# Performance work log

Measured on AMD Instinct MI355X. Metric: run time of the kernel, lower is better.

Reference implementation:

```python
import jax, jax.numpy as jnp
import numpy as np

EPS = 1e-8  # torch cosine_similarity norm clamp

def _cos(a, b, axis=-1):
    na = jnp.maximum(jnp.linalg.norm(a, axis=axis), EPS)
    nb = jnp.maximum(jnp.linalg.norm(b, axis=axis), EPS)
    return jnp.sum(a * b, axis=axis) / (na * nb)

def setup_inputs() -> dict:
    key = jax.random.key(0)
    ks = jax.random.split(key, 9)
    B, L, D, S = 8, 8192, 512, 131072
    scale = 0.02
    x = jax.random.normal(ks[0], (B, L, D), jnp.float32)
    context_W = jax.random.normal(ks[1], (D, D), jnp.float32) * scale
    context_b = jnp.zeros((D,), jnp.float32)
    pred_W1 = jax.random.normal(ks[2], (D, D), jnp.float32) * scale
    pred_b1 = jnp.zeros((D,), jnp.float32)
    pred_W2 = jax.random.normal(ks[3], (D, D), jnp.float32) * scale
    pred_b2 = jnp.zeros((D,), jnp.float32)
    raw_embeddings = jax.random.normal(ks[4], (S, D), jnp.float32)
    u = jax.random.uniform(ks[5], (S,), jnp.float32)
    surprise_level = jnp.where(u > 0.5, u, 0.0)  # ~half the slots active
    return {"x": x, "context_W": context_W, "context_b": context_b,
            "pred_W1": pred_W1, "pred_b1": pred_b1,
            "pred_W2": pred_W2, "pred_b2": pred_b2,
            "raw_embeddings": raw_embeddings, "surprise_level": surprise_level}

def reference(x, context_W, context_b, pred_W1, pred_b1, pred_W2, pred_b2,
              raw_embeddings, surprise_level):
    # context = pad(x[:, :-1], left-shift by one along seq), i.e. causal previous token
    context = jnp.pad(x[:, :-1, :], ((0, 0), (1, 0), (0, 0)))
    # predictor MLP on projected context (torch Linear: y = x @ W.T + b)
    ctx = context @ context_W.T + context_b
    h = jax.nn.gelu(ctx @ pred_W1.T + pred_b1, approximate=False)
    prediction = h @ pred_W2.T + pred_b2  # [B, L, D]
    mse = jnp.mean((x - prediction) ** 2, axis=-1)
    prediction_surprise = jnp.sqrt(mse)  # [B, L]

    # memory-contrastive surprise: cosine sim of pooled x vs active stored embeddings
    active = surprise_level > 0  # [S]
    x_pooled = jnp.mean(x, axis=1)  # [B, D]
    sim = _cos(x_pooled[:, None, :], raw_embeddings[None, :, :])  # [B, S]
    sim = jnp.where(active[None, :], sim, -jnp.inf)
    max_sim = jnp.max(sim, axis=-1)           # [B]
    best_idx = jnp.argmax(sim, axis=-1)       # [B]
    best_stored = raw_embeddings[best_idx]    # [B, D] argmax-based gather
    divergence = 1.0 - _cos(x, best_stored[:, None, :])  # [B, L]
    pattern_match = (max_sim[:, None] > 0.3).astype(x.dtype)
    contrastive = pattern_match * divergence

    surprise = jnp.maximum(prediction_surprise, contrastive * 2.0)  # [B, L]
    return surprise
```

## Files before the change

kernel.cpp:

```cpp
#include <hip/hip_runtime.h>
#include <math.h>

#define OFF_SIMKEY   0
#define OFF_POOLED   1024
#define ZEROED_BYTES 17408
#define OFF_MAXSIM   17408
#define OFF_NORME    17664
#define OFF_EBEST    17920
#define OFF_BPRIME   34304
#define OFF_WP       36864
#define OFF_W2B      561152

typedef __attribute__((ext_vector_type(8))) short bf16x8;
typedef __attribute__((ext_vector_type(4))) float f32x4;

__device__ inline unsigned short f2bf(float f) {
    unsigned int u = __float_as_uint(f);
    unsigned int r = (u + 0x7FFFu + ((u >> 16) & 1u)) >> 16;
    return (unsigned short)r;
}

__device__ inline void load_lds_16(const void* g, void* l) {
    __builtin_amdgcn_global_load_lds((const __attribute__((address_space(1))) void*)g,
                                     (__attribute__((address_space(3))) void*)l, 16, 0, 0);
}

__global__ void __launch_bounds__(256) k_pre(const float* __restrict__ W1, const float* __restrict__ Wc,
                      const float* __restrict__ b1, const float* __restrict__ bc,
                      unsigned short* __restrict__ Wp, float* __restrict__ bprime) {
    __shared__ float w1row[512];
    __shared__ float wsum[4];
    int t = threadIdx.x;
    int n = blockIdx.x >> 1, half = blockIdx.x & 1;
    if (t < 128) ((float4*)w1row)[t] = ((const float4*)(W1 + (size_t)n * 512))[t];
    __syncthreads();
    int k = half * 256 + t;
    float acc = 0.f;
#pragma unroll 8
    for (int j = 0; j < 512; ++j) acc += w1row[j] * Wc[(size_t)j * 512 + k];
    Wp[(size_t)n * 512 + k] = f2bf(acc);
    if (half == 0) {
        float p = w1row[t] * bc[t] + w1row[t + 256] * bc[t + 256];
#pragma unroll
        for (int m = 32; m >= 1; m >>= 1) p += __shfl_xor(p, m);
        if ((t & 63) == 0) wsum[t >> 6] = p;
        __syncthreads();
        if (t == 0) bprime[n] = b1[n] + wsum[0] + wsum[1] + wsum[2] + wsum[3];
    }
}

__global__ void __launch_bounds__(256) k_cast(const float* __restrict__ W2, unsigned short* __restrict__ W2b) {
    int i = blockIdx.x * 1024 + threadIdx.x * 4;
    float4 v = *(const float4*)(W2 + i);
    ushort4 o;
    o.x = f2bf(v.x); o.y = f2bf(v.y); o.z = f2bf(v.z); o.w = f2bf(v.w);
    *(ushort4*)(W2b + i) = o;
}

__global__ void __launch_bounds__(512) k_pool(const float* __restrict__ x, float* __restrict__ pooled) {
    int d = threadIdx.x;
    int b = blockIdx.y;
    int l0 = blockIdx.x * 128;
    const float* p = x + ((size_t)b * 8192 + l0) * 512 + d;
    float s = 0.f;
    for (int i = 0; i < 128; ++i) s += p[(size_t)i * 512];
    atomicAdd(&pooled[b * 512 + d], s);
}

__global__ void __launch_bounds__(256) k_sim(const float* __restrict__ E, const float* __restrict__ sl,
                     const float* __restrict__ pooledws, unsigned long long* __restrict__ simkey) {
    __shared__ float ps[4096];
    __shared__ unsigned long long wkey[4][8];
    int t = threadIdx.x, lane = t & 63, w = t >> 6;
#pragma unroll
    for (int c = 0; c < 16; ++c) ps[t + c * 256] = pooledws[t + c * 256] * (1.0f / 8192.0f);
    __syncthreads();
    float pr[8][8];
#pragma unroll
    for (int b = 0; b < 8; ++b) {
        float4 v0 = *(const float4*)&ps[b * 512 + lane * 8];
        float4 v1 = *(const float4*)&ps[b * 512 + lane * 8 + 4];
        pr[b][0] = v0.x; pr[b][1] = v0.y; pr[b][2] = v0.z; pr[b][3] = v0.w;
        pr[b][4] = v1.x; pr[b][5] = v1.y; pr[b][6] = v1.z; pr[b][7] = v1.w;
    }
    float npinv[8];
#pragma unroll
    for (int b = 0; b < 8; ++b) {
        float s = 0.f;
#pragma unroll
        for (int j = 0; j < 8; ++j) s += pr[b][j] * pr[b][j];
#pragma unroll
        for (int m = 32; m >= 1; m >>= 1) s += __shfl_xor(s, m);
        npinv[b] = 1.0f / fmaxf(sqrtf(s), 1e-8f);
    }
    unsigned long long best[8];
#pragma unroll
    for (int b = 0; b < 8; ++b) best[b] = 0ull;
    int sbase = blockIdx.x * 64 + w * 16;
    float mysl = (lane < 16) ? sl[sbase + lane] : 0.f;
    unsigned long long mask = __ballot(mysl > 0.0f);
    for (int it = 0; it < 16; ++it) {
        if (!((mask >> it) & 1ull)) continue;
        int s = sbase + it;
        const float4* ep = (const float4*)(E + (size_t)s * 512);
        float4 e0 = ep[lane * 2], e1 = ep[lane * 2 + 1];
        float nrm = e0.x * e0.x + e0.y * e0.y + e0.z * e0.z + e0.w * e0.w
                  + e1.x * e1.x + e1.y * e1.y + e1.z * e1.z + e1.w * e1.w;
        float dt[8];
#pragma unroll
        for (int b = 0; b < 8; ++b)
            dt[b] = e0.x * pr[b][0] + e0.y * pr[b][1] + e0.z * pr[b][2] + e0.w * pr[b][3]
                  + e1.x * pr[b][4] + e1.y * pr[b][5] + e1.z * pr[b][6] + e1.w * pr[b][7];
#pragma unroll
        for (int m = 32; m >= 1; m >>= 1) {
            nrm += __shfl_xor(nrm, m);
#pragma unroll
            for (int b = 0; b < 8; ++b) dt[b] += __shfl_xor(dt[b], m);
        }
        float neinv = 1.0f / fmaxf(sqrtf(nrm), 1e-8f);
#pragma unroll
        for (int b = 0; b < 8; ++b) {
            float sim = dt[b] * npinv[b] * neinv;
            unsigned int u = __float_as_uint(sim);
            unsigned int k32 = (u & 0x80000000u) ? ~u : (u | 0x80000000u);
            unsigned long long key = ((unsigned long long)k32 << 32) | (unsigned int)(~(unsigned int)s);
            if (key > best[b]) best[b] = key;
        }
    }
    if (lane == 0) {
#pragma unroll
        for (int b = 0; b < 8; ++b) wkey[w][b] = best[b];
    }
    __syncthreads();
    if (t < 8) {
        unsigned long long k = wkey[0][t];
#pragma unroll
        for (int w2 = 1; w2 < 4; ++w2) if (wkey[w2][t] > k) k = wkey[w2][t];
        if (k) atomicMax(&simkey[t], k);
    }
}

__global__ void __launch_bounds__(64) k_b2(const float* __restrict__ E, const unsigned long long* __restrict__ simkey,
                    float* __restrict__ max_sim, float* __restrict__ norm_e, float* __restrict__ ebest) {
    int b = blockIdx.x, lane = threadIdx.x;
    unsigned long long key = simkey[b];
    float ms; unsigned int idx;
    if (key == 0ull) { ms = -1e30f; idx = 0u; }
    else {
        unsigned int k32 = (unsigned int)(key >> 32);
        unsigned int u = (k32 & 0x80000000u) ? (k32 & 0x7FFFFFFFu) : ~k32;
        ms = __uint_as_float(u);
        idx = ~(unsigned int)(key & 0xFFFFFFFFull);
    }
    const float4* ep = (const float4*)(E + (size_t)idx * 512);
    float4 e0 = ep[lane * 2], e1 = ep[lane * 2 + 1];
    *(float4*)&ebest[b * 512 + lane * 8] = e0;
    *(float4*)&ebest[b * 512 + lane * 8 + 4] = e1;
    float s = e0.x * e0.x + e0.y * e0.y + e0.z * e0.z + e0.w * e0.w
            + e1.x * e1.x + e1.y * e1.y + e1.z * e1.z + e1.w * e1.w;
#pragma unroll
    for (int m = 32; m >= 1; m >>= 1) s += __shfl_xor(s, m);
    if (lane == 0) { max_sim[b] = ms; norm_e[b] = fmaxf(sqrtf(s), 1e-8f); }
}

__global__ void __launch_bounds__(256, 2) k_fused(
        const float* __restrict__ x, const unsigned short* __restrict__ Wp,
        const float* __restrict__ bprime, const unsigned short* __restrict__ W2b,
        const float* __restrict__ b2, const float* __restrict__ ebest,
        const float* __restrict__ max_sim, const float* __restrict__ norm_e,
        float* __restrict__ out) {
    __shared__ char smem[32768];
    unsigned short* Ts   = (unsigned short*)smem;
    unsigned short* Bs   = (unsigned short*)(smem + 5120);
    unsigned short* hbuf = (unsigned short*)(smem + 13312);
    float* red           = (float*)(smem + 30720);
    int t = threadIdx.x, lane = t & 63, w = t >> 6, l15 = lane & 15, quad = lane >> 4;
    int wr = w >> 1, wc = w & 1;
    const int gr0 = blockIdx.x * 64;
    const int b = gr0 >> 13;
    const int row0 = t >> 3, f4 = t & 7;

    ushort4 ush[16][2];
#pragma unroll
    for (int c = 0; c < 2; ++c) {
        int gr = gr0 + row0 + c * 32;
        bool z = ((gr & 8191) == 0);
        const float* src = x + ((size_t)gr - 1) * 512 + f4 * 4;
#pragma unroll
        for (int kt = 0; kt < 16; ++kt) {
            float4 v = make_float4(0.f, 0.f, 0.f, 0.f);
            if (!z) v = *(const float4*)(src + kt * 32);
            ushort4 o;
            o.x = f2bf(v.x); o.y = f2bf(v.y); o.z = f2bf(v.z); o.w = f2bf(v.w);
            ush[kt][c] = o;
        }
    }

    ushort4 hregs[16][2];
#pragma unroll
    for (int cb = 0; cb < 4; ++cb) {
        f32x4 acc[2][4];
#pragma unroll
        for (int i = 0; i < 2; ++i)
#pragma unroll
            for (int j = 0; j < 4; ++j) acc[i][j] = (f32x4){0.f, 0.f, 0.f, 0.f};
#pragma unroll
        for (int kt = 0; kt < 16; ++kt) {
            __syncthreads();
            *(ushort4*)&Ts[row0 * 40 + f4 * 4]        = ush[kt][0];
            *(ushort4*)&Ts[(row0 + 32) * 40 + f4 * 4] = ush[kt][1];
#pragma unroll
            for (int c = 0; c < 2; ++c) {
                int unit = c * 256 + w * 64 + lane;
                int row = unit >> 2, kb = unit & 3;
                load_lds_16(Wp + (size_t)(cb * 128 + row) * 512 + kt * 32 + kb * 8,
                            Bs + (size_t)(c * 256 + w * 64) * 8);
            }
            __syncthreads();
            bf16x8 af[2], bfr[4];
            af[0] = *(const bf16x8*)&Ts[(wr * 32 + l15) * 40 + quad * 8];
            af[1] = *(const bf16x8*)&Ts[(wr * 32 + 16 + l15) * 40 + quad * 8];
#pragma unroll
            for (int j = 0; j < 4; ++j)
                bfr[j] = *(const bf16x8*)&Bs[(wc * 64 + j * 16 + l15) * 32 + quad * 8];
#pragma unroll
            for (int i = 0; i < 2; ++i)
#pragma unroll
                for (int j = 0; j < 4; ++j)
                    acc[i][j] = __builtin_amdgcn_mfma_f32_16x16x32_bf16(af[i], bfr[j], acc[i][j], 0, 0, 0);
        }
        float bpj[4];
#pragma unroll
        for (int j = 0; j < 4; ++j) bpj[j] = bprime[cb * 128 + wc * 64 + j * 16 + l15];
#pragma unroll
        for (int i = 0; i < 2; ++i)
#pragma unroll
            for (int j = 0; j < 4; ++j)
#pragma unroll
                for (int r = 0; r < 4; ++r) {
                    int m = wr * 32 + i * 16 + quad * 4 + r;
                    int n = wc * 64 + j * 16 + l15;
                    float v = acc[i][j][r] + bpj[j];
                    v = 0.5f * v * (1.0f + erff(v * 0.70710678118f));
                    hbuf[m * 136 + n] = f2bf(v);
                }
        __syncthreads();
#pragma unroll
        for (int ktl = 0; ktl < 4; ++ktl) {
            hregs[cb * 4 + ktl][0] = *(const ushort4*)&hbuf[row0 * 136 + ktl * 32 + f4 * 4];
            hregs[cb * 4 + ktl][1] = *(const ushort4*)&hbuf[(row0 + 32) * 136 + ktl * 32 + f4 * 4];
        }
    }

    float psd[2][4], psx[2][4], pdt[2][4];
#pragma unroll
    for (int i = 0; i < 2; ++i)
#pragma unroll
        for (int r = 0; r < 4; ++r) { psd[i][r] = 0.f; psx[i][r] = 0.f; pdt[i][r] = 0.f; }
#pragma unroll
    for (int cb2 = 0; cb2 < 4; ++cb2) {
        f32x4 acc[2][4];
#pragma unroll
        for (int i = 0; i < 2; ++i)
#pragma unroll
            for (int j = 0; j < 4; ++j) acc[i][j] = (f32x4){0.f, 0.f, 0.f, 0.f};
#pragma unroll
        for (int kt = 0; kt < 16; ++kt) {
            __syncthreads();
            *(ushort4*)&Ts[row0 * 40 + f4 * 4]        = hregs[kt][0];
            *(ushort4*)&Ts[(row0 + 32) * 40 + f4 * 4] = hregs[kt][1];
#pragma unroll
            for (int c = 0; c < 2; ++c) {
                int unit = c * 256 + w * 64 + lane;
                int row = unit >> 2, kb = unit & 3;
                load_lds_16(W2b + (size_t)(cb2 * 128 + row) * 512 + kt * 32 + kb * 8,
                            Bs + (size_t)(c * 256 + w * 64) * 8);
            }
            __syncthreads();
            bf16x8 af[2], bfr[4];
            af[0] = *(const bf16x8*)&Ts[(wr * 32 + l15) * 40 + quad * 8];
            af[1] = *(const bf16x8*)&Ts[(wr * 32 + 16 + l15) * 40 + quad * 8];
#pragma unroll
            for (int j = 0; j < 4; ++j)
                bfr[j] = *(const bf16x8*)&Bs[(wc * 64 + j * 16 + l15) * 32 + quad * 8];
#pragma unroll
            for (int i = 0; i < 2; ++i)
#pragma unroll
                for (int j = 0; j < 4; ++j)
                    acc[i][j] = __builtin_amdgcn_mfma_f32_16x16x32_bf16(af[i], bfr[j], acc[i][j], 0, 0, 0);
        }
        float b2j[4], ej[4];
#pragma unroll
        for (int j = 0; j < 4; ++j) {
            int n = cb2 * 128 + wc * 64 + j * 16 + l15;
            b2j[j] = b2[n];
            ej[j] = ebest[b * 512 + n];
        }
#pragma unroll
        for (int i = 0; i < 2; ++i)
#pragma unroll
            for (int r = 0; r < 4; ++r) {
                int gr = gr0 + wr * 32 + i * 16 + quad * 4 + r;
#pragma unroll
                for (int j = 0; j < 4; ++j) {
                    int n = cb2 * 128 + wc * 64 + j * 16 + l15;
                    float p = acc[i][j][r] + b2j[j];
                    float xv = x[(size_t)gr * 512 + n];
                    float d = xv - p;
                    psd[i][r] += d * d; psx[i][r] += xv * xv; pdt[i][r] += xv * ej[j];
                }
            }
    }
#pragma unroll
    for (int i = 0; i < 2; ++i)
#pragma unroll
        for (int r = 0; r < 4; ++r) {
            float sd = psd[i][r], sx = psx[i][r], sdt = pdt[i][r];
#pragma unroll
            for (int m = 8; m >= 1; m >>= 1) {
                sd += __shfl_xor(sd, m);
                sx += __shfl_xor(sx, m);
                sdt += __shfl_xor(sdt, m);
            }
            if (l15 == 0) {
                int rl = i * 16 + quad * 4 + r;
                red[(w * 32 + rl) * 4 + 0] = sd;
                red[(w * 32 + rl) * 4 + 1] = sx;
                red[(w * 32 + rl) * 4 + 2] = sdt;
            }
        }
    __syncthreads();
    if (t < 64) {
        int rl = t & 31;
        int base = (t >> 5) * 2;
        float sd  = red[((base) * 32 + rl) * 4 + 0] + red[((base + 1) * 32 + rl) * 4 + 0];
        float sx  = red[((base) * 32 + rl) * 4 + 1] + red[((base + 1) * 32 + rl) * 4 + 1];
        float sdt = red[((base) * 32 + rl) * 4 + 2] + red[((base + 1) * 32 + rl) * 4 + 2];
        float ps = sqrtf(sd * (1.0f / 512.0f));
        float ms = max_sim[b];
        float c = 0.f;
        if (ms > 0.3f) {
            float nx = fmaxf(sqrtf(sx), 1e-8f);
            c = 2.0f * (1.0f - sdt / (nx * norm_e[b]));
        }
        out[gr0 + t] = fmaxf(ps, c);
    }
}

extern "C" void kernel_launch(void* const* d_in, const int* in_sizes, int n_in,
                              void* d_out, int out_size, void* d_ws, size_t ws_size,
                              hipStream_t stream) {
    const float* x  = (const float*)d_in[0];
    const float* Wc = (const float*)d_in[1];
    const float* bc = (const float*)d_in[2];
    const float* W1 = (const float*)d_in[3];
    const float* b1 = (const float*)d_in[4];
    const float* W2 = (const float*)d_in[5];
    const float* b2 = (const float*)d_in[6];
    const float* E  = (const float*)d_in[7];
    const float* sl = (const float*)d_in[8];

    char* ws = (char*)d_ws;
    unsigned long long* simkey = (unsigned long long*)(ws + OFF_SIMKEY);
    float* pooled  = (float*)(ws + OFF_POOLED);
    float* max_sim = (float*)(ws + OFF_MAXSIM);
    float* norm_e  = (float*)(ws + OFF_NORME);
    float* ebest   = (float*)(ws + OFF_EBEST);
    float* bprime  = (float*)(ws + OFF_BPRIME);
    unsigned short* Wp  = (unsigned short*)(ws + OFF_WP);
    unsigned short* W2b = (unsigned short*)(ws + OFF_W2B);
    float* out = (float*)d_out;

    hipMemsetAsync(ws, 0, ZEROED_BYTES, stream);
    k_pre<<<1024, 256, 0, stream>>>(W1, Wc, b1, bc, Wp, bprime);
    k_cast<<<256, 256, 0, stream>>>(W2, W2b);
    k_pool<<<dim3(64, 8), 512, 0, stream>>>(x, pooled);
    k_sim<<<2048, 256, 0, stream>>>(E, sl, pooled, simkey);
    k_b2<<<8, 64, 0, stream>>>(E, simkey, max_sim, norm_e, ebest);
    k_fused<<<1024, 256, 0, stream>>>(x, Wp, bprime, W2b, b2, ebest, max_sim, norm_e, out);
}
```

Before: 793.4 us.

## Compute full-width MLP per 64-row tile in one 1024-thread block with LDS-resident hidden

Replaces the 256-thread fused MLP kernel with a 1024-thread block that computes all 512 output columns of both GEMMs per 64-row tile. The GELU hidden activations stay in a 64KB LDS buffer instead of being round-tripped through registers and re-staged per column block. This cuts the k-loop iterations and barriers per tile from 64 to 16 per GEMM. It also vectorizes the pooling kernel with float4 loads and an in-block reduction before the atomics. The cost is about 112KB of LDS per block, so each CU likely holds only one block, and the launch bounds put pressure on registers.

```diff
diff --git a/kernel.cpp b/kernel.cpp
--- a/kernel.cpp
+++ b/kernel.cpp
@@ -58,13 +58,28 @@
 }
 
 __global__ void __launch_bounds__(512) k_pool(const float* __restrict__ x, float* __restrict__ pooled) {
-    int d = threadIdx.x;
+    __shared__ float4 pb[4][128];
+    int t = threadIdx.x;
+    int q = t & 127;
+    int rg = t >> 7;
     int b = blockIdx.y;
     int l0 = blockIdx.x * 128;
-    const float* p = x + ((size_t)b * 8192 + l0) * 512 + d;
-    float s = 0.f;
-    for (int i = 0; i < 128; ++i) s += p[(size_t)i * 512];
-    atomicAdd(&pooled[b * 512 + d], s);
+    const float4* p = (const float4*)(x + ((size_t)b * 8192 + l0 + rg) * 512) + q;
+    float4 s = make_float4(0.f, 0.f, 0.f, 0.f);
+#pragma unroll 8
+    for (int i = 0; i < 32; ++i) {
+        float4 v = p[(size_t)i * 512];
+        s.x += v.x; s.y += v.y; s.z += v.z; s.w += v.w;
+    }
+    pb[rg][q] = s;
+    __syncthreads();
+    if (rg == 0) {
+        float4 a = pb[0][q], b1_ = pb[1][q], c = pb[2][q], d = pb[3][q];
+        atomicAdd(&pooled[b * 512 + q * 4 + 0], a.x + b1_.x + c.x + d.x);
+        atomicAdd(&pooled[b * 512 + q * 4 + 1], a.y + b1_.y + c.y + d.y);
+        atomicAdd(&pooled[b * 512 + q * 4 + 2], a.z + b1_.z + c.z + d.z);
+        atomicAdd(&pooled[b * 512 + q * 4 + 3], a.w + b1_.w + c.w + d.w);
+    }
 }
 
 __global__ void __launch_bounds__(256) k_sim(const float* __restrict__ E, const float* __restrict__ sl,
@@ -163,179 +178,160 @@
     if (lane == 0) { max_sim[b] = ms; norm_e[b] = fmaxf(sqrtf(s), 1e-8f); }
 }
 
-__global__ void __launch_bounds__(256, 2) k_fused(
+__global__ void __launch_bounds__(1024, 4) k_mega(
         const float* __restrict__ x, const unsigned short* __restrict__ Wp,
         const float* __restrict__ bprime, const unsigned short* __restrict__ W2b,
         const float* __restrict__ b2, const float* __restrict__ ebest,
         const float* __restrict__ max_sim, const float* __restrict__ norm_e,
         float* __restrict__ out) {
-    __shared__ char smem[32768];
-    unsigned short* Ts   = (unsigned short*)smem;
-    unsigned short* Bs   = (unsigned short*)(smem + 5120);
-    unsigned short* hbuf = (unsigned short*)(smem + 13312);
-    float* red           = (float*)(smem + 30720);
-    int t = threadIdx.x, lane = t & 63, w = t >> 6, l15 = lane & 15, quad = lane >> 4;
-    int wr = w >> 1, wc = w & 1;
+    __shared__ char smem[114688];
+    unsigned short* Hs = (unsigned short*)(smem);
+    unsigned short* Bs = (unsigned short*)(smem + 65536);
+    unsigned short* Ts = (unsigned short*)(smem + 98304);
+    unsigned int*  Ts32 = (unsigned int*)Ts;
+    float* red = (float*)(smem + 102400);
+
+    const int t = threadIdx.x;
+    const int lane = t & 63, w = t >> 6;
+    const int l15 = lane & 15, quad = lane >> 4;
+    const int r = t >> 4, cp = t & 15;
     const int gr0 = blockIdx.x * 64;
     const int b = gr0 >> 13;
-    const int row0 = t >> 3, f4 = t & 7;
-
-    ushort4 ush[16][2];
-#pragma unroll
-    for (int c = 0; c < 2; ++c) {
-        int gr = gr0 + row0 + c * 32;
+
+    unsigned int areg[16];
+    {
+        int gr = gr0 + r;
         bool z = ((gr & 8191) == 0);
-        const float* src = x + ((size_t)gr - 1) * 512 + f4 * 4;
-#pragma unroll
-        for (int kt = 0; kt < 16; ++kt) {
-            float4 v = make_float4(0.f, 0.f, 0.f, 0.f);
-            if (!z) v = *(const float4*)(src + kt * 32);
-            ushort4 o;
-            o.x = f2bf(v.x); o.y = f2bf(v.y); o.z = f2bf(v.z); o.w = f2bf(v.w);
-            ush[kt][c] = o;
-        }
-    }
-
-    ushort4 hregs[16][2];
-#pragma unroll
-    for (int cb = 0; cb < 4; ++cb) {
-        f32x4 acc[2][4];
-#pragma unroll
-        for (int i = 0; i < 2; ++i)
-#pragma unroll
-            for (int j = 0; j < 4; ++j) acc[i][j] = (f32x4){0.f, 0.f, 0.f, 0.f};
-#pragma unroll
-        for (int kt = 0; kt < 16; ++kt) {
-            __syncthreads();
-            *(ushort4*)&Ts[row0 * 40 + f4 * 4]        = ush[kt][0];
-            *(ushort4*)&Ts[(row0 + 32) * 40 + f4 * 4] = ush[kt][1];
-#pragma unroll
-            for (int c = 0; c < 2; ++c) {
-                int unit = c * 256 + w * 64 + lane;
-                int row = unit >> 2, kb = unit & 3;
-                load_lds_16(Wp + (size_t)(cb * 128 + row) * 512 + kt * 32 + kb * 8,
-                            Bs + (size_t)(c * 256 + w * 64) * 8);
-            }
-            __syncthreads();
-            bf16x8 af[2], bfr[4];
-            af[0] = *(const bf16x8*)&Ts[(wr * 32 + l15) * 40 + quad * 8];
-            af[1] = *(const bf16x8*)&Ts[(wr * 32 + 16 + l15) * 40 + quad * 8];
-#pragma unroll
-            for (int j = 0; j < 4; ++j)
-                bfr[j] = *(const bf16x8*)&Bs[(wc * 64 + j * 16 + l15) * 32 + quad * 8];
-#pragma unroll
-            for (int i = 0; i < 2; ++i)
-#pragma unroll
-                for (int j = 0; j < 4; ++j)
-                    acc[i][j] = __builtin_amdgcn_mfma_f32_16x16x32_bf16(af[i], bfr[j], acc[i][j], 0, 0, 0);
-        }
-        float bpj[4];
-#pragma unroll
-        for (int j = 0; j < 4; ++j) bpj[j] = bprime[cb * 128 + wc * 64 + j * 16 + l15];
-#pragma unroll
-        for (int i = 0; i < 2; ++i)
-#pragma unroll
-            for (int j = 0; j < 4; ++j)
-#pragma unroll
-                for (int r = 0; r < 4; ++r) {
-                    int m = wr * 32 + i * 16 + quad * 4 + r;
-                    int n = wc * 64 + j * 16 + l15;
-                    float v = acc[i][j][r] + bpj[j];
+        const float* src = x + ((size_t)gr - 1) * 512 + cp * 2;
+#pragma unroll
+        for (int k = 0; k < 16; ++k) {
+            float2 v = make_float2(0.f, 0.f);
+            if (!z) v = *(const float2*)(src + k * 32);
+            areg[k] = (unsigned int)f2bf(v.x) | ((unsigned int)f2bf(v.y) << 16);
+        }
+    }
+
+    f32x4 acc[4][2];
+#pragma unroll
+    for (int i = 0; i < 4; ++i)
+#pragma unroll
+        for (int j = 0; j < 2; ++j) acc[i][j] = (f32x4){0.f, 0.f, 0.f, 0.f};
+#pragma unroll
+    for (int kt = 0; kt < 16; ++kt) {
+        __syncthreads();
+        Ts32[r * 16 + cp] = areg[kt];
+#pragma unroll
+        for (int c = 0; c < 2; ++c) {
+            int unit = c * 1024 + t;
+            load_lds_16(Wp + (size_t)(unit >> 2) * 512 + kt * 32 + (unit & 3) * 8,
+                        Bs + c * 8192 + w * 512);
+        }
+        __syncthreads();
+        bf16x8 af[4], bfr[2];
+#pragma unroll
+        for (int i = 0; i < 4; ++i)
+            af[i] = *(const bf16x8*)&Ts[(i * 16 + l15) * 32 + quad * 8];
+#pragma unroll
+        for (int j = 0; j < 2; ++j)
+            bfr[j] = *(const bf16x8*)&Bs[(w * 32 + j * 16 + l15) * 32 + quad * 8];
+#pragma unroll
+        for (int i = 0; i < 4; ++i)
+#pragma unroll
+            for (int j = 0; j < 2; ++j)
+                acc[i][j] = __builtin_amdgcn_mfma_f32_16x16x32_bf16(af[i], bfr[j], acc[i][j], 0, 0, 0);
+    }
+    {
+        float bpj[2];
+#pragma unroll
+        for (int j = 0; j < 2; ++j) bpj[j] = bprime[w * 32 + j * 16 + l15];
+#pragma unroll
+        for (int i = 0; i < 4; ++i)
+#pragma unroll
+            for (int j = 0; j < 2; ++j)
+#pragma unroll
+                for (int rg = 0; rg < 4; ++rg) {
+                    int m = i * 16 + quad * 4 + rg;
+                    int n = w * 32 + j * 16 + l15;
+                    float v = acc[i][j][rg] + bpj[j];
                     v = 0.5f * v * (1.0f + erff(v * 0.70710678118f));
-                    hbuf[m * 136 + n] = f2bf(v);
+                    Hs[(n >> 5) * 2048 + m * 32 + (n & 31)] = f2bf(v);
                 }
-        __syncthreads();
-#pragma unroll
-        for (int ktl = 0; ktl < 4; ++ktl) {
-            hregs[cb * 4 + ktl][0] = *(const ushort4*)&hbuf[row0 * 136 + ktl * 32 + f4 * 4];
-            hregs[cb * 4 + ktl][1] = *(const ushort4*)&hbuf[(row0 + 32) * 136 + ktl * 32 + f4 * 4];
-        }
-    }
-
-    float psd[2][4], psx[2][4], pdt[2][4];
-#pragma unroll
-    for (int i = 0; i < 2; ++i)
-#pragma unroll
-        for (int r = 0; r < 4; ++r) { psd[i][r] = 0.f; psx[i][r] = 0.f; pdt[i][r] = 0.f; }
-#pragma unroll
-    for (int cb2 = 0; cb2 < 4; ++cb2) {
-        f32x4 acc[2][4];
-#pragma unroll
-        for (int i = 0; i < 2; ++i)
-#pragma unroll
-            for (int j = 0; j < 4; ++j) acc[i][j] = (f32x4){0.f, 0.f, 0.f, 0.f};
-#pragma unroll
-        for (int kt = 0; kt < 16; ++kt) {
-            __syncthreads();
-            *(ushort4*)&Ts[row0 * 40 + f4 * 4]        = hregs[kt][0];
-            *(ushort4*)&Ts[(row0 + 32) * 40 + f4 * 4] = hregs[kt][1];
-#pragma unroll
-            for (int c = 0; c < 2; ++c) {
-                int unit = c * 256 + w * 64 + lane;
-                int row = unit >> 2, kb = unit & 3;
-                load_lds_16(W2b + (size_t)(cb2 * 128 + row) * 512 + kt * 32 + kb * 8,
-                            Bs + (size_t)(c * 256 + w * 64) * 8);
-            }
-            __syncthreads();
-            bf16x8 af[2], bfr[4];
-            af[0] = *(const bf16x8*)&Ts[(wr * 32 + l15) * 40 + quad * 8];
-            af[1] = *(const bf16x8*)&Ts[(wr * 32 + 16 + l15) * 40 + quad * 8];
-#pragma unroll
-            for (int j = 0; j < 4; ++j)
-                bfr[j] = *(const bf16x8*)&Bs[(wc * 64 + j * 16 + l15) * 32 + quad * 8];
-#pragma unroll
-            for (int i = 0; i < 2; ++i)
-#pragma unroll
-                for (int j = 0; j < 4; ++j)
-                    acc[i][j] = __builtin_amdgcn_mfma_f32_16x16x32_bf16(af[i], bfr[j], acc[i][j], 0, 0, 0);
-        }
-        float b2j[4], ej[4];
-#pragma unroll
-        for (int j = 0; j < 4; ++j) {
-            int n = cb2 * 128 + wc * 64 + j * 16 + l15;
+    }
+
+    f32x4 acc2[4][2];
+#pragma unroll
+    for (int i = 0; i < 4; ++i)
+#pragma unroll
+        for (int j = 0; j < 2; ++j) acc2[i][j] = (f32x4){0.f, 0.f, 0.f, 0.f};
+#pragma unroll
+    for (int kt = 0; kt < 16; ++kt) {
+        __syncthreads();
+#pragma unroll
+        for (int c = 0; c < 2; ++c) {
+            int unit = c * 1024 + t;
+            load_lds_16(W2b + (size_t)(unit >> 2) * 512 + kt * 32 + (unit & 3) * 8,
+                        Bs + c * 8192 + w * 512);
+        }
+        __syncthreads();
+        bf16x8 af[4], bfr[2];
+#pragma unroll
+        for (int i = 0; i < 4; ++i)
+            af[i] = *(const bf16x8*)&Hs[kt * 2048 + (i * 16 + l15) * 32 + quad * 8];
+#pragma unroll
+        for (int j = 0; j < 2; ++j)
+            bfr[j] = *(const bf16x8*)&Bs[(w * 32 + j * 16 + l15) * 32 + quad * 8];
+#pragma unroll
+        for (int i = 0; i < 4; ++i)
+#pragma unroll
+            for (int j = 0; j < 2; ++j)
+                acc2[i][j] = __builtin_amdgcn_mfma_f32_16x16x32_bf16(af[i], bfr[j], acc2[i][j], 0, 0, 0);
+    }
+
+    {
+        float b2j[2], ej[2];
+#pragma unroll
+        for (int j = 0; j < 2; ++j) {
+            int n = w * 32 + j * 16 + l15;
             b2j[j] = b2[n];
             ej[j] = ebest[b * 512 + n];
         }
 #pragma unroll
-        for (int i = 0; i < 2; ++i)
-#pragma unroll
-            for (int r = 0; r < 4; ++r) {
-                int gr = gr0 + wr * 32 + i * 16 + quad * 4 + r;
-#pragma unroll
-                for (int j = 0; j < 4; ++j) {
-                    int n = cb2 * 128 + wc * 64 + j * 16 + l15;
-                    float p = acc[i][j][r] + b2j[j];
+        for (int i = 0; i < 4; ++i)
+#pragma unroll
+            for (int rg = 0; rg < 4; ++rg) {
+                int m = i * 16 + quad * 4 + rg;
+                int gr = gr0 + m;
+                float sd = 0.f, sx = 0.f, sdt = 0.f;
+#pragma unroll
+                for (int j = 0; j < 2; ++j) {
+                    int n = w * 32 + j * 16 + l15;
+                    float p = acc2[i][j][rg] + b2j[j];
                     float xv = x[(size_t)gr * 512 + n];
                     float d = xv - p;
-                    psd[i][r] += d * d; psx[i][r] += xv * xv; pdt[i][r] += xv * ej[j];
+                    sd += d * d; sx += xv * xv; sdt += xv * ej[j];
+                }
+#pragma unroll
+                for (int mm = 8; mm >= 1; mm >>= 1) {
+                    sd += __shfl_xor(sd, mm);
+                    sx += __shfl_xor(sx, mm);
+                    sdt += __shfl_xor(sdt, mm);
+                }
+                if (l15 == 0) {
+                    red[(m * 16 + w) * 3 + 0] = sd;
+                    red[(m * 16 + w) * 3 + 1] = sx;
+                    red[(m * 16 + w) * 3 + 2] = sdt;
                 }
             }
     }
-#pragma unroll
-    for (int i = 0; i < 2; ++i)
-#pragma unroll
-        for (int r = 0; r < 4; ++r) {
-            float sd = psd[i][r], sx = psx[i][r], sdt = pdt[i][r];
-#pragma unroll
-            for (int m = 8; m >= 1; m >>= 1) {
-                sd += __shfl_xor(sd, m);
-                sx += __shfl_xor(sx, m);
-                sdt += __shfl_xor(sdt, m);
-            }
-            if (l15 == 0) {
-                int rl = i * 16 + quad * 4 + r;
-                red[(w * 32 + rl) * 4 + 0] = sd;
-                red[(w * 32 + rl) * 4 + 1] = sx;
-                red[(w * 32 + rl) * 4 + 2] = sdt;
-            }
-        }
     __syncthreads();
     if (t < 64) {
-        int rl = t & 31;
-        int base = (t >> 5) * 2;
-        float sd  = red[((base) * 32 + rl) * 4 + 0] + red[((base + 1) * 32 + rl) * 4 + 0];
-        float sx  = red[((base) * 32 + rl) * 4 + 1] + red[((base + 1) * 32 + rl) * 4 + 1];
-        float sdt = red[((base) * 32 + rl) * 4 + 2] + red[((base + 1) * 32 + rl) * 4 + 2];
+        float sd = 0.f, sx = 0.f, sdt = 0.f;
+#pragma unroll
+        for (int w2 = 0; w2 < 16; ++w2) {
+            sd  += red[(t * 16 + w2) * 3 + 0];
+            sx  += red[(t * 16 + w2) * 3 + 1];
+            sdt += red[(t * 16 + w2) * 3 + 2];
+        }
         float ps = sqrtf(sd * (1.0f / 512.0f));
         float ms = max_sim[b];
         float c = 0.f;
@@ -377,5 +373,5 @@
     k_pool<<<dim3(64, 8), 512, 0, stream>>>(x, pooled);
     k_sim<<<2048, 256, 0, stream>>>(E, sl, pooled, simkey);
     k_b2<<<8, 64, 0, stream>>>(E, simkey, max_sim, norm_e, ebest);
-    k_fused<<<1024, 256, 0, stream>>>(x, Wp, bprime, W2b, b2, ebest, max_sim, norm_e, out);
-}
+    k_mega<<<1024, 1024, 0, stream>>>(x, Wp, bprime, W2b, b2, ebest, max_sim, norm_e, out);
+}
```

After: 705.3 us. 11.1% less time.
